# Performance work log

Measured on AMD Instinct MI355X. Metric: run time of the kernel, lower is better.

## Reference

```python
import jax, jax.numpy as jnp
import numpy as np

EPS_NORM = 1e-12  # torch F.normalize clamp_min eps
EPS_LOG = 1e-10


def setup_inputs() -> dict:
    key = jax.random.key(0)
    k1, k2 = jax.random.split(key)
    N, D = 12288, 128
    embeddings = jax.random.uniform(k1, (N, D), dtype=jnp.float32)
    adj = jax.random.uniform(k2, (N, N), dtype=jnp.float32)
    lambda_reg = jnp.float32(1.0)
    return {"embeddings": embeddings, "adj": adj, "lambda_reg": lambda_reg}


def reference(embeddings, adj, lambda_reg):
    # F.normalize(embeddings, dim=1, p=4): x / max(||x||_4, eps)
    norm4 = jnp.power(jnp.sum(jnp.abs(embeddings) ** 4, axis=1, keepdims=True), 0.25)
    e = embeddings / jnp.maximum(norm4, EPS_NORM)          # [N, D]
    log_p = jnp.log(e + EPS_LOG)                           # [N, D]
    p_log_p = jnp.sum(e * log_p, axis=1)                   # [N]
    cross = e @ log_p.T                                    # [N, N]
    kl = p_log_p[:, None] - cross                          # [N, N]
    # F.normalize(adj, p=1, dim=1): row-wise L1 normalization
    adj_n = adj / jnp.maximum(jnp.sum(jnp.abs(adj), axis=1, keepdims=True), EPS_NORM)
    return lambda_reg * jnp.sum(kl * adj_n)
```

## Files before the change

### kernel.cpp

```cpp
#include <hip/hip_runtime.h>
#include <hip/hip_bf16.h>

#define EPSN 1e-12f
#define EPSL 1e-10f
#define TILEM 32
#define KSPLIT 2
#define KS 256

typedef __attribute__((ext_vector_type(8))) short short8;
typedef __attribute__((ext_vector_type(4))) float f32x4;

__device__ __forceinline__ unsigned short f2bf_rne(float f) {
  union { float f; unsigned u; } x; x.f = f;
  unsigned r = x.u + 0x7FFFu + ((x.u >> 16) & 1u);
  return (unsigned short)(r >> 16);
}

__global__ __launch_bounds__(256)
void prep_kernel(const float* __restrict__ emb, float* __restrict__ eC,
                 unsigned short* __restrict__ lpB, float* __restrict__ plp,
                 float* __restrict__ S, float* __restrict__ v, int N) {
  int w = threadIdx.x >> 6, l = threadIdx.x & 63;
  int row = blockIdx.x * 4 + w;
  if (row >= N) return;
  const float* x = emb + (size_t)row * 128;
  float2 xv = *(const float2*)(x + 2 * l);
  float s4 = xv.x*xv.x*xv.x*xv.x + xv.y*xv.y*xv.y*xv.y;
  #pragma unroll
  for (int m = 1; m < 64; m <<= 1) s4 += __shfl_xor(s4, m);
  float denom = fmaxf(sqrtf(sqrtf(s4)), EPSN);
  float e0 = xv.x / denom, e1 = xv.y / denom;
  float lp0 = logf(e0 + EPSL), lp1 = logf(e1 + EPSL);
  int Rg = row >> 4, lhig = (row >> 2) & 3, rg = row & 3;
  int d0 = 2 * l, d1 = 2 * l + 1;
  eC[(((size_t)Rg * 8 + (d0 >> 4)) * 64 + (d0 & 15) + 16 * lhig) * 4 + rg] = e0;
  eC[(((size_t)Rg * 8 + (d1 >> 4)) * 64 + (d1 & 15) + 16 * lhig) * 4 + rg] = e1;
  int ksr = row >> 5, lhir = (row >> 3) & 3, jr = row & 7;
  lpB[((size_t)(ksr*8 + (d0>>4))*64 + (d0&15) + 16*lhir)*8 + jr] = f2bf_rne(lp0);
  lpB[((size_t)(ksr*8 + (d1>>4))*64 + (d1&15) + 16*lhir)*8 + jr] = f2bf_rne(lp1);
  float pl = e0 * lp0 + e1 * lp1;
  #pragma unroll
  for (int m = 1; m < 64; m <<= 1) pl += __shfl_xor(pl, m);
  if (l == 0) { plp[row] = pl; S[row] = 0.f; v[row] = 0.f; }
}

__global__ __launch_bounds__(256, 3)
void gemm_kernel(const float* __restrict__ adj, const float* __restrict__ eC,
                 const unsigned short* __restrict__ lpB,
                 float* __restrict__ S, float* __restrict__ v, int N) {
  __shared__ unsigned short ash[2][TILEM * KS];
  int w = threadIdx.x >> 6, l = threadIdx.x & 63;
  int l16 = l & 15, lhi = l >> 4;
  int row0 = blockIdx.x * TILEM;
  int kr = N / KSPLIT;
  int k0 = blockIdx.y * kr;
  int nt = kr / KS;

  f32x4 acc[2][2];
  #pragma unroll
  for (int i = 0; i < 2; ++i)
    #pragma unroll
    for (int j = 0; j < 2; ++j) acc[i][j] = (f32x4){0.f, 0.f, 0.f, 0.f};
  float sAcc[8];
  #pragma unroll
  for (int j = 0; j < 8; ++j) sAcc[j] = 0.f;

  const float* aBase = adj + (size_t)(row0 + 8 * w) * N + k0 + 4 * l;
  float4 ar[8];

#define LOADA(t)                                                        \
  {                                                                     \
    _Pragma("unroll")                                                   \
    for (int j_ = 0; j_ < 8; ++j_)                                      \
      ar[j_] = *(const float4*)(aBase + (size_t)j_ * N + (size_t)(t) * KS); \
  }

#define STAGE(bi)                                                       \
  {                                                                     \
    char* base_ = (char*)ash[bi];                                       \
    _Pragma("unroll")                                                   \
    for (int j_ = 0; j_ < 8; ++j_) {                                    \
      float4 x_ = ar[j_];                                               \
      sAcc[j_] += (x_.x + x_.y) + (x_.z + x_.w);                        \
      unsigned p0_ = (unsigned)f2bf_rne(x_.x) | ((unsigned)f2bf_rne(x_.y) << 16); \
      unsigned p1_ = (unsigned)f2bf_rne(x_.z) | ((unsigned)f2bf_rne(x_.w) << 16); \
      int rl_ = 8 * w + j_;                                             \
      int off_ = rl_ * 512 + ((l * 8) ^ ((rl_ & 7) << 4));              \
      *(uint2*)(base_ + off_) = make_uint2(p0_, p1_);                   \
    }                                                                   \
  }

#define MSTEP(bi, t)                                                    \
  {                                                                     \
    const char* base_ = (const char*)ash[bi];                           \
    size_t fb_ = (size_t)((k0 + (t) * KS) >> 5) * 8;                    \
    _Pragma("unroll")                                                   \
    for (int kg_ = 0; kg_ < 8; ++kg_) {                                 \
      int ao_ = (kg_ * 64 + lhi * 16) ^ ((l16 & 7) << 4);               \
      short8 a0_ = *(const short8*)(base_ + l16 * 512 + ao_);           \
      short8 a1_ = *(const short8*)(base_ + (16 + l16) * 512 + ao_);    \
      short8 b0_ = ((const short8*)lpB)[(fb_ + (size_t)kg_ * 8 + 2 * w) * 64 + l];     \
      short8 b1_ = ((const short8*)lpB)[(fb_ + (size_t)kg_ * 8 + 2 * w + 1) * 64 + l]; \
      acc[0][0] = __builtin_amdgcn_mfma_f32_16x16x32_bf16(a0_, b0_, acc[0][0], 0, 0, 0); \
      acc[0][1] = __builtin_amdgcn_mfma_f32_16x16x32_bf16(a0_, b1_, acc[0][1], 0, 0, 0); \
      acc[1][0] = __builtin_amdgcn_mfma_f32_16x16x32_bf16(a1_, b0_, acc[1][0], 0, 0, 0); \
      acc[1][1] = __builtin_amdgcn_mfma_f32_16x16x32_bf16(a1_, b1_, acc[1][1], 0, 0, 0); \
    }                                                                   \
  }

  LOADA(0);
  STAGE(0);
  __syncthreads();

  for (int t = 0; t < nt; ++t) {
    if (t + 1 < nt) LOADA(t + 1);
    MSTEP(t & 1, t);
    if (t + 1 < nt) STAGE((t + 1) & 1);
    __syncthreads();
  }

  #pragma unroll
  for (int j = 0; j < 8; ++j) {
    float s = sAcc[j];
    #pragma unroll
    for (int m = 1; m < 64; m <<= 1) s += __shfl_xor(s, m);
    if (l == 0) atomicAdd(&S[row0 + 8 * w + j], s);
  }

  #pragma unroll
  for (int rt = 0; rt < 2; ++rt) {
    int R = (row0 >> 4) + rt;
    float p0 = 0.f, p1 = 0.f, p2 = 0.f, p3 = 0.f;
    #pragma unroll
    for (int c = 0; c < 2; ++c) {
      int ctg = 2 * w + c;
      float4 ef = *(const float4*)(eC + (((size_t)R * 8 + ctg) * 64 + l) * 4);
      p0 += ef.x * acc[rt][c][0];
      p1 += ef.y * acc[rt][c][1];
      p2 += ef.z * acc[rt][c][2];
      p3 += ef.w * acc[rt][c][3];
    }
    #pragma unroll
    for (int m = 1; m < 16; m <<= 1) {
      p0 += __shfl_xor(p0, m);
      p1 += __shfl_xor(p1, m);
      p2 += __shfl_xor(p2, m);
      p3 += __shfl_xor(p3, m);
    }
    if (l16 == 0) {
      int rb = row0 + rt * 16 + lhi * 4;
      atomicAdd(&v[rb + 0], p0);
      atomicAdd(&v[rb + 1], p1);
      atomicAdd(&v[rb + 2], p2);
      atomicAdd(&v[rb + 3], p3);
    }
  }
}

__global__ __launch_bounds__(1024)
void final_kernel(const float* __restrict__ plp, const float* __restrict__ S,
                  const float* __restrict__ v, const float* __restrict__ lam,
                  float* __restrict__ out, int N) {
  __shared__ float red[16];
  float acc = 0.f;
  for (int i = threadIdx.x; i < N; i += 1024) {
    float s = S[i], d = fmaxf(s, EPSN);
    acc += plp[i] * (s / d) - v[i] / d;
  }
  #pragma unroll
  for (int m = 1; m < 64; m <<= 1) acc += __shfl_xor(acc, m);
  int w = threadIdx.x >> 6, l = threadIdx.x & 63;
  if (l == 0) red[w] = acc;
  __syncthreads();
  if (threadIdx.x == 0) {
    float t = 0.f;
    #pragma unroll
    for (int i = 0; i < 16; ++i) t += red[i];
    out[0] = lam[0] * t;
  }
}

extern "C" void kernel_launch(void* const* d_in, const int* in_sizes, int n_in,
                              void* d_out, int out_size, void* d_ws, size_t ws_size,
                              hipStream_t stream) {
  const float* emb = (const float*)d_in[0];
  const float* adj = (const float*)d_in[1];
  const float* lam = (const float*)d_in[2];
  int N = in_sizes[0] / 128;

  char* ws = (char*)d_ws;
  float* eC           = (float*)ws;
  unsigned short* lpB = (unsigned short*)(ws + (size_t)N * 512);
  float* plp          = (float*)(ws + (size_t)N * 768);
  float* S            = plp + N;
  float* v            = S + N;

  prep_kernel<<<(N + 3) / 4, 256, 0, stream>>>(emb, eC, lpB, plp, S, v, N);
  dim3 grid(N / TILEM, KSPLIT);
  gemm_kernel<<<grid, 256, 0, stream>>>(adj, eC, lpB, S, v, N);
  final_kernel<<<1, 1024, 0, stream>>>(plp, S, v, lam, (float*)d_out, N);
}
```

Baseline: 221.3 us.

## Use 64-row tiles with 16-way K split, unrolled pipeline and nontemporal adj loads

The gemm kernel now uses 64-row tiles instead of 32, and splits K 16 ways instead of 2. Each block therefore processes only three 256-wide chunks in a fully unrolled pipeline. The B fragments are prefetched into registers ahead of each compute step, and adj is read with nontemporal loads to avoid polluting the cache. The goal is better B reuse per loaded A row and more blocks in flight to saturate HBM bandwidth on the adj stream. In exchange the kernel uses many more registers and issues eight times more atomics to S and v, and it hardcodes N=12288 in the K-split calculation.

```diff
diff --git a/kernel.cpp b/kernel.cpp
--- a/kernel.cpp
+++ b/kernel.cpp
@@ -3,17 +3,16 @@
 
 #define EPSN 1e-12f
 #define EPSL 1e-10f
-#define TILEM 32
-#define KSPLIT 2
-#define KS 256
+#define KSPLIT 16
+#define CHK 256
 
 typedef __attribute__((ext_vector_type(8))) short short8;
 typedef __attribute__((ext_vector_type(4))) float f32x4;
 
-__device__ __forceinline__ unsigned short f2bf_rne(float f) {
+__device__ __forceinline__ unsigned f2bf(float f) {
   union { float f; unsigned u; } x; x.f = f;
   unsigned r = x.u + 0x7FFFu + ((x.u >> 16) & 1u);
-  return (unsigned short)(r >> 16);
+  return r >> 16;
 }
 
 __global__ __launch_bounds__(256)
@@ -36,109 +35,121 @@
   eC[(((size_t)Rg * 8 + (d0 >> 4)) * 64 + (d0 & 15) + 16 * lhig) * 4 + rg] = e0;
   eC[(((size_t)Rg * 8 + (d1 >> 4)) * 64 + (d1 & 15) + 16 * lhig) * 4 + rg] = e1;
   int ksr = row >> 5, lhir = (row >> 3) & 3, jr = row & 7;
-  lpB[((size_t)(ksr*8 + (d0>>4))*64 + (d0&15) + 16*lhir)*8 + jr] = f2bf_rne(lp0);
-  lpB[((size_t)(ksr*8 + (d1>>4))*64 + (d1&15) + 16*lhir)*8 + jr] = f2bf_rne(lp1);
+  lpB[((size_t)(ksr*8 + (d0>>4))*64 + (d0&15) + 16*lhir)*8 + jr] = (unsigned short)f2bf(lp0);
+  lpB[((size_t)(ksr*8 + (d1>>4))*64 + (d1&15) + 16*lhir)*8 + jr] = (unsigned short)f2bf(lp1);
   float pl = e0 * lp0 + e1 * lp1;
   #pragma unroll
   for (int m = 1; m < 64; m <<= 1) pl += __shfl_xor(pl, m);
   if (l == 0) { plp[row] = pl; S[row] = 0.f; v[row] = 0.f; }
 }
 
-__global__ __launch_bounds__(256, 3)
+__global__ __launch_bounds__(256)
 void gemm_kernel(const float* __restrict__ adj, const float* __restrict__ eC,
                  const unsigned short* __restrict__ lpB,
                  float* __restrict__ S, float* __restrict__ v, int N) {
-  __shared__ unsigned short ash[2][TILEM * KS];
+  __shared__ unsigned short ash[2][64 * CHK];
   int w = threadIdx.x >> 6, l = threadIdx.x & 63;
   int l16 = l & 15, lhi = l >> 4;
-  int row0 = blockIdx.x * TILEM;
-  int kr = N / KSPLIT;
-  int k0 = blockIdx.y * kr;
-  int nt = kr / KS;
-
-  f32x4 acc[2][2];
-  #pragma unroll
-  for (int i = 0; i < 2; ++i)
-    #pragma unroll
-    for (int j = 0; j < 2; ++j) acc[i][j] = (f32x4){0.f, 0.f, 0.f, 0.f};
-  float sAcc[8];
-  #pragma unroll
-  for (int j = 0; j < 8; ++j) sAcc[j] = 0.f;
-
-  const float* aBase = adj + (size_t)(row0 + 8 * w) * N + k0 + 4 * l;
-  float4 ar[8];
+  int row0 = blockIdx.x * 64;
+  int k0 = blockIdx.y * (12288 / KSPLIT);
+
+  f32x4 acc[4][2];
+  #pragma unroll
+  for (int i = 0; i < 4; ++i) {
+    acc[i][0] = (f32x4){0.f, 0.f, 0.f, 0.f};
+    acc[i][1] = (f32x4){0.f, 0.f, 0.f, 0.f};
+  }
+  float sAcc[16];
+  #pragma unroll
+  for (int j = 0; j < 16; ++j) sAcc[j] = 0.f;
+
+  const float* aBase = adj + (size_t)(row0 + 16 * w) * N + k0 + 4 * l;
+  f32x4 ar[16];
+  short8 bb[2][8];
 
 #define LOADA(t)                                                        \
   {                                                                     \
     _Pragma("unroll")                                                   \
-    for (int j_ = 0; j_ < 8; ++j_)                                      \
-      ar[j_] = *(const float4*)(aBase + (size_t)j_ * N + (size_t)(t) * KS); \
+    for (int j_ = 0; j_ < 16; ++j_)                                     \
+      ar[j_] = __builtin_nontemporal_load(                              \
+          (const f32x4*)(aBase + (size_t)j_ * N + (t) * CHK));          \
+  }
+
+#define LOADB(t)                                                        \
+  {                                                                     \
+    size_t fb_ = (size_t)((k0 + (t) * CHK) >> 5) * 8;                   \
+    _Pragma("unroll")                                                   \
+    for (int kg_ = 0; kg_ < 8; ++kg_) {                                 \
+      bb[0][kg_] = ((const short8*)lpB)[(fb_ + kg_*8 + 2*w    ) * 64 + l]; \
+      bb[1][kg_] = ((const short8*)lpB)[(fb_ + kg_*8 + 2*w + 1) * 64 + l]; \
+    }                                                                   \
   }
 
 #define STAGE(bi)                                                       \
   {                                                                     \
-    char* base_ = (char*)ash[bi];                                       \
-    _Pragma("unroll")                                                   \
-    for (int j_ = 0; j_ < 8; ++j_) {                                    \
-      float4 x_ = ar[j_];                                               \
-      sAcc[j_] += (x_.x + x_.y) + (x_.z + x_.w);                        \
-      unsigned p0_ = (unsigned)f2bf_rne(x_.x) | ((unsigned)f2bf_rne(x_.y) << 16); \
-      unsigned p1_ = (unsigned)f2bf_rne(x_.z) | ((unsigned)f2bf_rne(x_.w) << 16); \
-      int rl_ = 8 * w + j_;                                             \
-      int off_ = rl_ * 512 + ((l * 8) ^ ((rl_ & 7) << 4));              \
-      *(uint2*)(base_ + off_) = make_uint2(p0_, p1_);                   \
+    char* q_ = (char*)ash[bi];                                          \
+    _Pragma("unroll")                                                   \
+    for (int j_ = 0; j_ < 16; ++j_) {                                   \
+      f32x4 x_ = ar[j_];                                                \
+      sAcc[j_] += (x_[0] + x_[1]) + (x_[2] + x_[3]);                    \
+      unsigned p0_ = f2bf(x_[0]) | (f2bf(x_[1]) << 16);                 \
+      unsigned p1_ = f2bf(x_[2]) | (f2bf(x_[3]) << 16);                 \
+      int rl_ = 16 * w + j_;                                            \
+      *(uint2*)(q_ + rl_ * 512 + ((8 * l) ^ ((rl_ & 7) << 4))) =        \
+          make_uint2(p0_, p1_);                                         \
     }                                                                   \
   }
 
-#define MSTEP(bi, t)                                                    \
+#define COMP(bi)                                                        \
   {                                                                     \
     const char* base_ = (const char*)ash[bi];                           \
-    size_t fb_ = (size_t)((k0 + (t) * KS) >> 5) * 8;                    \
+    int xr_ = (l16 & 7) << 4;                                           \
     _Pragma("unroll")                                                   \
     for (int kg_ = 0; kg_ < 8; ++kg_) {                                 \
-      int ao_ = (kg_ * 64 + lhi * 16) ^ ((l16 & 7) << 4);               \
-      short8 a0_ = *(const short8*)(base_ + l16 * 512 + ao_);           \
-      short8 a1_ = *(const short8*)(base_ + (16 + l16) * 512 + ao_);    \
-      short8 b0_ = ((const short8*)lpB)[(fb_ + (size_t)kg_ * 8 + 2 * w) * 64 + l];     \
-      short8 b1_ = ((const short8*)lpB)[(fb_ + (size_t)kg_ * 8 + 2 * w + 1) * 64 + l]; \
-      acc[0][0] = __builtin_amdgcn_mfma_f32_16x16x32_bf16(a0_, b0_, acc[0][0], 0, 0, 0); \
-      acc[0][1] = __builtin_amdgcn_mfma_f32_16x16x32_bf16(a0_, b1_, acc[0][1], 0, 0, 0); \
-      acc[1][0] = __builtin_amdgcn_mfma_f32_16x16x32_bf16(a1_, b0_, acc[1][0], 0, 0, 0); \
-      acc[1][1] = __builtin_amdgcn_mfma_f32_16x16x32_bf16(a1_, b1_, acc[1][1], 0, 0, 0); \
+      int off_ = (kg_ * 64 + lhi * 16) ^ xr_;                           \
+      short8 a0_ = *(const short8*)(base_ + (l16     ) * 512 + off_);   \
+      short8 a1_ = *(const short8*)(base_ + (l16 + 16) * 512 + off_);   \
+      short8 a2_ = *(const short8*)(base_ + (l16 + 32) * 512 + off_);   \
+      short8 a3_ = *(const short8*)(base_ + (l16 + 48) * 512 + off_);   \
+      acc[0][0] = __builtin_amdgcn_mfma_f32_16x16x32_bf16(a0_, bb[0][kg_], acc[0][0], 0, 0, 0); \
+      acc[0][1] = __builtin_amdgcn_mfma_f32_16x16x32_bf16(a0_, bb[1][kg_], acc[0][1], 0, 0, 0); \
+      acc[1][0] = __builtin_amdgcn_mfma_f32_16x16x32_bf16(a1_, bb[0][kg_], acc[1][0], 0, 0, 0); \
+      acc[1][1] = __builtin_amdgcn_mfma_f32_16x16x32_bf16(a1_, bb[1][kg_], acc[1][1], 0, 0, 0); \
+      acc[2][0] = __builtin_amdgcn_mfma_f32_16x16x32_bf16(a2_, bb[0][kg_], acc[2][0], 0, 0, 0); \
+      acc[2][1] = __builtin_amdgcn_mfma_f32_16x16x32_bf16(a2_, bb[1][kg_], acc[2][1], 0, 0, 0); \
+      acc[3][0] = __builtin_amdgcn_mfma_f32_16x16x32_bf16(a3_, bb[0][kg_], acc[3][0], 0, 0, 0); \
+      acc[3][1] = __builtin_amdgcn_mfma_f32_16x16x32_bf16(a3_, bb[1][kg_], acc[3][1], 0, 0, 0); \
     }                                                                   \
   }
 
-  LOADA(0);
-  STAGE(0);
-  __syncthreads();
-
-  for (int t = 0; t < nt; ++t) {
-    if (t + 1 < nt) LOADA(t + 1);
-    MSTEP(t & 1, t);
-    if (t + 1 < nt) STAGE((t + 1) & 1);
-    __syncthreads();
-  }
-
-  #pragma unroll
-  for (int j = 0; j < 8; ++j) {
+  LOADA(0); STAGE(0);
+  __syncthreads();
+  LOADB(0); LOADA(1); COMP(0); STAGE(1);
+  __syncthreads();
+  LOADB(1); LOADA(2); COMP(1); STAGE(0);
+  __syncthreads();
+  LOADB(2); COMP(0);
+
+  #pragma unroll
+  for (int j = 0; j < 16; ++j) {
     float s = sAcc[j];
     #pragma unroll
     for (int m = 1; m < 64; m <<= 1) s += __shfl_xor(s, m);
-    if (l == 0) atomicAdd(&S[row0 + 8 * w + j], s);
-  }
-
-  #pragma unroll
-  for (int rt = 0; rt < 2; ++rt) {
+    if (l == 0) atomicAdd(&S[row0 + 16 * w + j], s);
+  }
+
+  #pragma unroll
+  for (int rt = 0; rt < 4; ++rt) {
     int R = (row0 >> 4) + rt;
     float p0 = 0.f, p1 = 0.f, p2 = 0.f, p3 = 0.f;
     #pragma unroll
     for (int c = 0; c < 2; ++c) {
-      int ctg = 2 * w + c;
-      float4 ef = *(const float4*)(eC + (((size_t)R * 8 + ctg) * 64 + l) * 4);
-      p0 += ef.x * acc[rt][c][0];
-      p1 += ef.y * acc[rt][c][1];
-      p2 += ef.z * acc[rt][c][2];
-      p3 += ef.w * acc[rt][c][3];
+      int ct = 2 * w + c;
+      f32x4 ef = *(const f32x4*)(eC + (((size_t)R * 8 + ct) * 64 + l) * 4);
+      p0 += ef[0] * acc[rt][c][0];
+      p1 += ef[1] * acc[rt][c][1];
+      p2 += ef[2] * acc[rt][c][2];
+      p3 += ef[3] * acc[rt][c][3];
     }
     #pragma unroll
     for (int m = 1; m < 16; m <<= 1) {
@@ -196,7 +207,7 @@
   float* v            = S + N;
 
   prep_kernel<<<(N + 3) / 4, 256, 0, stream>>>(emb, eC, lpB, plp, S, v, N);
-  dim3 grid(N / TILEM, KSPLIT);
+  dim3 grid(N / 64, KSPLIT);
   gemm_kernel<<<grid, 256, 0, stream>>>(adj, eC, lpB, S, v, N);
   final_kernel<<<1, 1024, 0, stream>>>(plp, S, v, lam, (float*)d_out, N);
 }
```

Result: slower. 233.4 us (+5.4%).
